# Kernel optimization log

Measured on AMD Instinct MI355X. Metric: run time of the kernel, lower is better.

Reference implementation:

```python
import jax, jax.numpy as jnp
import numpy as np

B, L, H, NH, NB = 8, 200, 128, 4, 2
HD = H // NH
ITEM_NUM, TIME_SPAN = 50000, 256
PAD = -2.0**32 + 1.0


def setup_inputs() -> dict:
    key = jax.random.key(0)
    ks = jax.random.split(key, 32)
    def g(i, shape, s=0.02):
        return jax.random.normal(ks[i], shape, jnp.float32) * s
    item_emb = g(0, (ITEM_NUM + 1, H)).at[0].set(0.0)  # padding_idx=0
    return dict(
        user_ids=jax.random.randint(ks[1], (B,), 0, 1000),
        log_seqs=jax.random.randint(ks[2], (B, L), 0, ITEM_NUM),
        time_matrices=jax.random.randint(ks[3], (B, L, L), 0, TIME_SPAN + 1),
        pos_seqs=jax.random.randint(ks[4], (B, L), 0, ITEM_NUM + 1),
        neg_seqs=jax.random.randint(ks[5], (B, L), 0, ITEM_NUM + 1),
        item_emb=item_emb,
        pos_K_emb=g(6, (L, H)), pos_V_emb=g(7, (L, H)),
        time_K_emb=g(8, (TIME_SPAN + 1, H)), time_V_emb=g(9, (TIME_SPAN + 1, H)),
        attn_ln_g=jnp.ones((NB, H)), attn_ln_b=jnp.zeros((NB, H)),
        Wq=g(10, (NB, H, H)), bq=jnp.zeros((NB, H)),
        Wk=g(11, (NB, H, H)), bk=jnp.zeros((NB, H)),
        Wv=g(12, (NB, H, H)), bv=jnp.zeros((NB, H)),
        fwd_ln_g=jnp.ones((NB, H)), fwd_ln_b=jnp.zeros((NB, H)),
        W1=g(13, (NB, H, H)), b1=jnp.zeros((NB, H)),
        W2=g(14, (NB, H, H)), b2=jnp.zeros((NB, H)),
        last_ln_g=jnp.ones((H,)), last_ln_b=jnp.zeros((H,)),
    )


def _ln(x, g, b, eps=1e-8):
    m = x.mean(-1, keepdims=True)
    v = jnp.var(x, axis=-1, keepdims=True)
    return (x - m) / jnp.sqrt(v + eps) * g + b


def _heads(x):
    # [..., H] -> [NH, ..., HD]; matches torch.cat(torch.split(x, HD, -1), 0)
    y = x.reshape(x.shape[:-1] + (NH, HD))
    return jnp.moveaxis(y, -2, 0)


def reference(user_ids, log_seqs, time_matrices, pos_seqs, neg_seqs, item_emb,
              pos_K_emb, pos_V_emb, time_K_emb, time_V_emb,
              attn_ln_g, attn_ln_b, Wq, bq, Wk, bk, Wv, bv,
              fwd_ln_g, fwd_ln_b, W1, b1, W2, b2, last_ln_g, last_ln_b):
    # user_ids is unused in the original forward as well.
    tmask = log_seqs == 0                                  # [B,L] True = pad
    keep = (~tmask)[..., None].astype(jnp.float32)
    seqs = item_emb[log_seqs] * np.float32(np.sqrt(H))
    seqs = seqs * keep
    pKh = _heads(pos_K_emb)                                # [NH,L,HD]
    pVh = _heads(pos_V_emb)
    tKh = _heads(time_K_emb[time_matrices])                # [NH,B,L,L,HD]
    tVh = _heads(time_V_emb[time_matrices])
    causal = ~jnp.tril(jnp.ones((L, L), bool))             # True above diag -> masked
    bad = tmask[:, :, None] | causal[None]                 # [B,L,L]
    scale = np.float32(np.sqrt(HD))
    for i in range(NB):
        Qin = _ln(seqs, attn_ln_g[i], attn_ln_b[i])
        Qh = _heads(Qin @ Wq[i].T + bq[i])                 # [NH,B,L,HD]
        Kh = _heads(seqs @ Wk[i].T + bk[i])
        Vh = _heads(seqs @ Wv[i].T + bv[i])
        attn = (jnp.einsum('nbqd,nbkd->nbqk', Qh, Kh)
                + jnp.einsum('nbqd,nkd->nbqk', Qh, pKh)
                + jnp.einsum('nbqkd,nbqd->nbqk', tKh, Qh)) / scale
        attn = jnp.where(bad[None], PAD, attn)
        attn = jax.nn.softmax(attn, axis=-1)
        out = (jnp.einsum('nbqk,nbkd->nbqd', attn, Vh)
               + jnp.einsum('nbqk,nkd->nbqd', attn, pVh)
               + jnp.einsum('nbqk,nbqkd->nbqd', attn, tVh))
        out = jnp.moveaxis(out, 0, -2).reshape(seqs.shape)  # merge heads -> [B,L,H]
        seqs = Qin + out                                    # residual uses LN'd Q (as in source)
        seqs = _ln(seqs, fwd_ln_g[i], fwd_ln_b[i])
        ff = jax.nn.relu(seqs @ W1[i].T + b1[i]) @ W2[i].T + b2[i] + seqs
        seqs = ff * keep
    log_feats = _ln(seqs, last_ln_g, last_ln_b)
    pos_logits = (log_feats * item_emb[pos_seqs]).sum(-1)   # [B,L]
    neg_logits = (log_feats * item_emb[neg_seqs]).sum(-1)
    return pos_logits, neg_logits
```

## Files before the change

### kernel.cpp

```cpp
#include <hip/hip_runtime.h>
#include <hip/hip_bf16.h>

#define BB 8
#define LL 200
#define HH 128
#define NHEAD 4
#define HDIM 32
#define NBLK 2
#define BL (BB * LL)
#define NT 257
#define QT 8
#define NQT 25
#define SSP 208
#define KTP 66
#define ASP 36
#define BSP 66
#define FASP 20
#define RSP 132

static constexpr float SQRT_H    = 11.313708498984761f;
static constexpr float INV_SCALE = 0.17677669529663687f;
static constexpr float PADV      = -4294967295.0f;

__global__ void k_qkv_gemm(const float* __restrict__ seqs_in,
                           const int* __restrict__ log_seqs,
                           const float* __restrict__ item_emb,
                           const float* __restrict__ g, const float* __restrict__ bia,
                           const float* __restrict__ Wq, const float* __restrict__ bq,
                           const float* __restrict__ Wk, const float* __restrict__ bk,
                           const float* __restrict__ Wv, const float* __restrict__ bv,
                           const float* __restrict__ posK, const float* __restrict__ posV,
                           float* __restrict__ Qin, float* __restrict__ Q,
                           float* __restrict__ K, float* __restrict__ V) {
    int mt = blockIdx.x / 6, nt = blockIdx.x % 6;
    int matsel = nt >> 1;
    int jb = (nt & 1) * 64;
    int row0 = mt * 32;
    int tid = threadIdx.x;
    __shared__ float As[128 * ASP];
    __shared__ float Bs[128 * BSP];

    {
        int r = tid >> 3, seg = tid & 7;
        int row = row0 + r;
        float4 vv[4];
        if (seqs_in) {
            #pragma unroll
            for (int i = 0; i < 4; i++)
                vv[i] = *(const float4*)(seqs_in + (size_t)row * HH + seg * 16 + i * 4);
        } else {
            int idx = log_seqs[row];
            if (idx == 0) {
                #pragma unroll
                for (int i = 0; i < 4; i++) vv[i] = make_float4(0.f, 0.f, 0.f, 0.f);
            } else {
                #pragma unroll
                for (int i = 0; i < 4; i++) {
                    float4 e = *(const float4*)(item_emb + (size_t)idx * HH + seg * 16 + i * 4);
                    vv[i] = make_float4(e.x * SQRT_H, e.y * SQRT_H, e.z * SQRT_H, e.w * SQRT_H);
                }
            }
        }
        if (matsel == 0) {
            float s = 0.f, s2 = 0.f;
            #pragma unroll
            for (int i = 0; i < 4; i++) {
                s  += vv[i].x + vv[i].y + vv[i].z + vv[i].w;
                s2 += vv[i].x * vv[i].x + vv[i].y * vv[i].y + vv[i].z * vv[i].z + vv[i].w * vv[i].w;
            }
            #pragma unroll
            for (int off = 1; off < 8; off <<= 1) {
                s  += __shfl_xor(s, off);
                s2 += __shfl_xor(s2, off);
            }
            float mean = s * (1.f / HH);
            float var  = s2 * (1.f / HH) - mean * mean;
            float inv  = 1.f / sqrtf(var + 1e-8f);
            #pragma unroll
            for (int i = 0; i < 4; i++) {
                int k = seg * 16 + i * 4;
                float4 g4 = *(const float4*)(g + k);
                float4 b4 = *(const float4*)(bia + k);
                float4 y;
                y.x = (vv[i].x - mean) * inv * g4.x + b4.x;
                y.y = (vv[i].y - mean) * inv * g4.y + b4.y;
                y.z = (vv[i].z - mean) * inv * g4.z + b4.z;
                y.w = (vv[i].w - mean) * inv * g4.w + b4.w;
                As[(k + 0) * ASP + r] = y.x;
                As[(k + 1) * ASP + r] = y.y;
                As[(k + 2) * ASP + r] = y.z;
                As[(k + 3) * ASP + r] = y.w;
                if (nt == 0) *(float4*)(Qin + (size_t)row * HH + k) = y;
            }
        } else {
            #pragma unroll
            for (int i = 0; i < 4; i++) {
                int k = seg * 16 + i * 4;
                As[(k + 0) * ASP + r] = vv[i].x;
                As[(k + 1) * ASP + r] = vv[i].y;
                As[(k + 2) * ASP + r] = vv[i].z;
                As[(k + 3) * ASP + r] = vv[i].w;
            }
        }
    }
    {
        const float* W = (matsel == 0) ? Wq : (matsel == 1) ? Wk : Wv;
        int k4 = tid & 31, jj0 = tid >> 5;
        #pragma unroll
        for (int p = 0; p < 8; p++) {
            int jj = jj0 + p * 8;
            float4 w = *(const float4*)(W + (size_t)(jb + jj) * HH + k4 * 4);
            Bs[(k4 * 4 + 0) * BSP + jj] = w.x;
            Bs[(k4 * 4 + 1) * BSP + jj] = w.y;
            Bs[(k4 * 4 + 2) * BSP + jj] = w.z;
            Bs[(k4 * 4 + 3) * BSP + jj] = w.w;
        }
    }
    __syncthreads();

    int my = tid >> 5, jx = tid & 31;
    float a00=0,a01=0,a10=0,a11=0,a20=0,a21=0,a30=0,a31=0;
    #pragma unroll 4
    for (int k = 0; k < HH; k++) {
        float4 a = *(const float4*)&As[k * ASP + my * 4];
        float2 b = *(const float2*)&Bs[k * BSP + jx * 2];
        a00 += a.x * b.x; a01 += a.x * b.y;
        a10 += a.y * b.x; a11 += a.y * b.y;
        a20 += a.z * b.x; a21 += a.z * b.y;
        a30 += a.w * b.x; a31 += a.w * b.y;
    }
    float accs[4][2] = {{a00,a01},{a10,a11},{a20,a21},{a30,a31}};
    int col = jb + jx * 2;
    if (matsel == 0) {
        float2 bb = *(const float2*)(bq + col);
        #pragma unroll
        for (int r = 0; r < 4; r++) {
            int row = row0 + my * 4 + r;
            float2 o = make_float2((accs[r][0] + bb.x) * INV_SCALE,
                                   (accs[r][1] + bb.y) * INV_SCALE);
            *(float2*)(Q + (size_t)row * HH + col) = o;
        }
    } else if (matsel == 1) {
        float2 bb = *(const float2*)(bk + col);
        #pragma unroll
        for (int r = 0; r < 4; r++) {
            int row = row0 + my * 4 + r;
            int l = row % LL;
            float2 pk = *(const float2*)(posK + (size_t)l * HH + col);
            float2 o = make_float2(accs[r][0] + bb.x + pk.x, accs[r][1] + bb.y + pk.y);
            *(float2*)(K + (size_t)row * HH + col) = o;
        }
    } else {
        float2 bb = *(const float2*)(bv + col);
        #pragma unroll
        for (int r = 0; r < 4; r++) {
            int row = row0 + my * 4 + r;
            int l = row % LL;
            float2 pv = *(const float2*)(posV + (size_t)l * HH + col);
            float2 o = make_float2(accs[r][0] + bb.x + pv.x, accs[r][1] + bb.y + pv.y);
            *(float2*)(V + (size_t)row * HH + col) = o;
        }
    }
}

__global__ void k_attn(const float* __restrict__ Q, const float* __restrict__ K,
                       const float* __restrict__ V,
                       const float* __restrict__ timeK, const float* __restrict__ timeV,
                       const int* __restrict__ tm,
                       float* __restrict__ att) {
    int bn = blockIdx.x & 31;
    int b = bn >> 2, n = bn & 3;
    int qt = (NQT - 1) - (blockIdx.x >> 5);
    int q0 = qt * QT;
    int kmax = q0 + QT - 1;
    int tid = threadIdx.x;
    int wv = tid >> 6, ln = tid & 63;

    __shared__ float Qs[QT * HDIM];
    __shared__ float KstT[HDIM * KTP];
    __shared__ float DTW[QT * NT];
    __shared__ float Ssc[QT * SSP];
    __shared__ int   tmst[QT * LL];
    __shared__ float Ost[QT * HDIM];

    Ost[tid] = 0.f;
    if (tid < 64) {
        int qi = tid >> 3, d4 = tid & 7;
        *(float4*)(Qs + qi * HDIM + d4 * 4) =
            *(const float4*)(Q + ((size_t)(b * LL + q0 + qi)) * HH + n * HDIM + d4 * 4);
    }
    #pragma unroll
    for (int qi = 0; qi < QT; qi++)
        if (tid < LL)
            tmst[qi * LL + tid] = tm[((size_t)(b * LL + q0 + qi)) * LL + tid];
    __syncthreads();

    int k2 = tid & 31, qi_c = tid >> 5;

    for (int c = 0; c < 5; c++) {
        #pragma unroll
        for (int p = 0; p < 2; p++) {
            int idx = tid + p * 256;
            int r = idx >> 3, d4 = idx & 7;
            int tau = c * 64 + r;
            float4 w = make_float4(0.f, 0.f, 0.f, 0.f);
            if (tau < NT) w = *(const float4*)(timeK + (size_t)tau * HH + n * HDIM + d4 * 4);
            KstT[(d4 * 4 + 0) * KTP + r] = w.x;
            KstT[(d4 * 4 + 1) * KTP + r] = w.y;
            KstT[(d4 * 4 + 2) * KTP + r] = w.z;
            KstT[(d4 * 4 + 3) * KTP + r] = w.w;
        }
        __syncthreads();
        float a0 = 0.f, a1 = 0.f;
        #pragma unroll 4
        for (int d = 0; d < HDIM; d++) {
            float qv = Qs[qi_c * HDIM + d];
            float2 kv = *(const float2*)&KstT[d * KTP + k2 * 2];
            a0 += qv * kv.x; a1 += qv * kv.y;
        }
        int tau0 = c * 64 + k2 * 2;
        if (tau0 < NT)     DTW[qi_c * NT + tau0]     = a0;
        if (tau0 + 1 < NT) DTW[qi_c * NT + tau0 + 1] = a1;
        __syncthreads();
    }

    int nch = (kmax >> 6) + 1;
    for (int c = 0; c < nch; c++) {
        #pragma unroll
        for (int p = 0; p < 2; p++) {
            int idx = tid + p * 256;
            int r = idx >> 3, d4 = idx & 7;
            int k = c * 64 + r;
            float4 w = make_float4(0.f, 0.f, 0.f, 0.f);
            if (k < LL) w = *(const float4*)(K + ((size_t)(b * LL + k)) * HH + n * HDIM + d4 * 4);
            KstT[(d4 * 4 + 0) * KTP + r] = w.x;
            KstT[(d4 * 4 + 1) * KTP + r] = w.y;
            KstT[(d4 * 4 + 2) * KTP + r] = w.z;
            KstT[(d4 * 4 + 3) * KTP + r] = w.w;
        }
        __syncthreads();
        float a0 = 0.f, a1 = 0.f;
        #pragma unroll 4
        for (int d = 0; d < HDIM; d++) {
            float qv = Qs[qi_c * HDIM + d];
            float2 kv = *(const float2*)&KstT[d * KTP + k2 * 2];
            a0 += qv * kv.x; a1 += qv * kv.y;
        }
        int q = q0 + qi_c;
        int k0 = c * 64 + k2 * 2;
        if (k0 <= kmax)
            Ssc[qi_c * SSP + k0] = (k0 <= q) ? (a0 + DTW[qi_c * NT + tmst[qi_c * LL + k0]]) : PADV;
        if (k0 + 1 <= kmax)
            Ssc[qi_c * SSP + k0 + 1] = (k0 + 1 <= q) ? (a1 + DTW[qi_c * NT + tmst[qi_c * LL + k0 + 1]]) : PADV;
        __syncthreads();
    }

    for (int idx = tid; idx < QT * NT; idx += 256) DTW[idx] = 0.f;
    __syncthreads();

    for (int rr = 0; rr < 2; rr++) {
        int qi = wv + rr * 4;
        int q = q0 + qi;
        float sv[4];
        float m = PADV;
        #pragma unroll
        for (int jj = 0; jj < 4; jj++) {
            int k = ln + 64 * jj;
            sv[jj] = (k <= q) ? Ssc[qi * SSP + k] : PADV;
            m = fmaxf(m, sv[jj]);
        }
        for (int off = 32; off; off >>= 1) m = fmaxf(m, __shfl_xor(m, off));
        float sum = 0.f;
        #pragma unroll
        for (int jj = 0; jj < 4; jj++) {
            int k = ln + 64 * jj;
            sv[jj] = (k <= q) ? __expf(sv[jj] - m) : 0.f;
            sum += sv[jj];
        }
        for (int off = 32; off; off >>= 1) sum += __shfl_xor(sum, off);
        float inv = 1.f / sum;
        #pragma unroll
        for (int jj = 0; jj < 4; jj++) {
            int k = ln + 64 * jj;
            float p = sv[jj] * inv;
            if (k < SSP) Ssc[qi * SSP + k] = (k <= q) ? p : 0.f;
            if (k <= q) atomicAdd(&DTW[qi * NT + tmst[qi * LL + k]], p);
        }
    }
    __syncthreads();

    int d = tid & 31, kg = tid >> 5;
    float acc[QT] = {0,0,0,0,0,0,0,0};
    const float* vb = V + ((size_t)(b * LL)) * HH + n * HDIM + d;
    for (int k = kg; k <= kmax; k += 8) {
        float v = vb[(size_t)k * HH];
        #pragma unroll
        for (int qi = 0; qi < QT; qi++) acc[qi] += Ssc[qi * SSP + k] * v;
    }
    const float* tvb = timeV + n * HDIM + d;
    for (int t = kg; t < NT; t += 8) {
        float v = tvb[(size_t)t * HH];
        #pragma unroll
        for (int qi = 0; qi < QT; qi++) acc[qi] += DTW[qi * NT + t] * v;
    }
    #pragma unroll
    for (int qi = 0; qi < QT; qi++) atomicAdd(&Ost[qi * HDIM + d], acc[qi]);
    __syncthreads();
    {
        int qi = tid >> 5;
        att[((size_t)(b * LL + q0 + qi)) * HH + n * HDIM + d] = Ost[qi * HDIM + d];
    }
}

__global__ void k_ff1(const float* __restrict__ Qin, const float* __restrict__ att,
                      const float* __restrict__ g, const float* __restrict__ bia,
                      const float* __restrict__ W1, const float* __restrict__ b1,
                      float* __restrict__ h1) {
    int mt = blockIdx.x >> 1, nt = blockIdx.x & 1;
    int jb = nt * 64;
    int row0 = mt * 16;
    int tid = threadIdx.x;
    __shared__ float As[128 * FASP];
    __shared__ float Bs[128 * BSP];

    {
        int r = tid >> 4, seg = tid & 15;
        int row = row0 + r;
        float4 vv[2];
        #pragma unroll
        for (int i = 0; i < 2; i++) {
            int k = seg * 8 + i * 4;
            float4 q4 = *(const float4*)(Qin + (size_t)row * HH + k);
            float4 a4 = *(const float4*)(att + (size_t)row * HH + k);
            vv[i] = make_float4(q4.x + a4.x, q4.y + a4.y, q4.z + a4.z, q4.w + a4.w);
        }
        float s = 0.f, s2 = 0.f;
        #pragma unroll
        for (int i = 0; i < 2; i++) {
            s  += vv[i].x + vv[i].y + vv[i].z + vv[i].w;
            s2 += vv[i].x * vv[i].x + vv[i].y * vv[i].y + vv[i].z * vv[i].z + vv[i].w * vv[i].w;
        }
        #pragma unroll
        for (int off = 1; off < 16; off <<= 1) {
            s  += __shfl_xor(s, off);
            s2 += __shfl_xor(s2, off);
        }
        float mean = s * (1.f / HH);
        float var  = s2 * (1.f / HH) - mean * mean;
        float inv  = 1.f / sqrtf(var + 1e-8f);
        #pragma unroll
        for (int i = 0; i < 2; i++) {
            int k = seg * 8 + i * 4;
            float4 g4 = *(const float4*)(g + k);
            float4 b4 = *(const float4*)(bia + k);
            As[(k + 0) * FASP + r] = (vv[i].x - mean) * inv * g4.x + b4.x;
            As[(k + 1) * FASP + r] = (vv[i].y - mean) * inv * g4.y + b4.y;
            As[(k + 2) * FASP + r] = (vv[i].z - mean) * inv * g4.z + b4.z;
            As[(k + 3) * FASP + r] = (vv[i].w - mean) * inv * g4.w + b4.w;
        }
    }
    {
        int k4 = tid & 31, jj0 = tid >> 5;
        #pragma unroll
        for (int p = 0; p < 8; p++) {
            int jj = jj0 + p * 8;
            float4 w = *(const float4*)(W1 + (size_t)(jb + jj) * HH + k4 * 4);
            Bs[(k4 * 4 + 0) * BSP + jj] = w.x;
            Bs[(k4 * 4 + 1) * BSP + jj] = w.y;
            Bs[(k4 * 4 + 2) * BSP + jj] = w.z;
            Bs[(k4 * 4 + 3) * BSP + jj] = w.w;
        }
    }
    __syncthreads();

    int my = tid >> 5, jx = tid & 31;
    float a00 = 0, a01 = 0, a10 = 0, a11 = 0;
    #pragma unroll 4
    for (int k = 0; k < HH; k++) {
        float2 a = *(const float2*)&As[k * FASP + my * 2];
        float2 b = *(const float2*)&Bs[k * BSP + jx * 2];
        a00 += a.x * b.x; a01 += a.x * b.y;
        a10 += a.y * b.x; a11 += a.y * b.y;
    }
    int col = jb + jx * 2;
    float2 bb = *(const float2*)(b1 + col);
    {
        int row = row0 + my * 2;
        float2 o0 = make_float2(fmaxf(a00 + bb.x, 0.f), fmaxf(a01 + bb.y, 0.f));
        float2 o1 = make_float2(fmaxf(a10 + bb.x, 0.f), fmaxf(a11 + bb.y, 0.f));
        *(float2*)(h1 + (size_t)row * HH + col) = o0;
        *(float2*)(h1 + (size_t)(row + 1) * HH + col) = o1;
    }
}

__global__ void k_ff2(const float* __restrict__ h1,
                      const float* __restrict__ Qin, const float* __restrict__ att,
                      const float* __restrict__ g, const float* __restrict__ bia,
                      const float* __restrict__ W2, const float* __restrict__ b2,
                      const int* __restrict__ log_seqs,
                      float* __restrict__ out) {
    int mt = blockIdx.x >> 1, nt = blockIdx.x & 1;
    int jb = nt * 64;
    int row0 = mt * 16;
    int tid = threadIdx.x;
    __shared__ float As[128 * FASP];
    __shared__ float Bs[128 * BSP];
    __shared__ float Rs[16 * RSP];
    __shared__ float mu[16], rstd[16];

    {
        int r = tid >> 4, seg = tid & 15;
        int row = row0 + r;
        #pragma unroll
        for (int i = 0; i < 2; i++) {
            int k = seg * 8 + i * 4;
            float4 h4 = *(const float4*)(h1 + (size_t)row * HH + k);
            As[(k + 0) * FASP + r] = h4.x;
            As[(k + 1) * FASP + r] = h4.y;
            As[(k + 2) * FASP + r] = h4.z;
            As[(k + 3) * FASP + r] = h4.w;
        }
        float s = 0.f, s2 = 0.f;
        #pragma unroll
        for (int i = 0; i < 2; i++) {
            int k = seg * 8 + i * 4;
            float4 q4 = *(const float4*)(Qin + (size_t)row * HH + k);
            float4 a4 = *(const float4*)(att + (size_t)row * HH + k);
            float4 v = make_float4(q4.x + a4.x, q4.y + a4.y, q4.z + a4.z, q4.w + a4.w);
            *(float4*)(Rs + r * RSP + k) = v;
            s  += v.x + v.y + v.z + v.w;
            s2 += v.x * v.x + v.y * v.y + v.z * v.z + v.w * v.w;
        }
        #pragma unroll
        for (int off = 1; off < 16; off <<= 1) {
            s  += __shfl_xor(s, off);
            s2 += __shfl_xor(s2, off);
        }
        float mean = s * (1.f / HH);
        float var  = s2 * (1.f / HH) - mean * mean;
        if (seg == 0) { mu[r] = mean; rstd[r] = 1.f / sqrtf(var + 1e-8f); }
    }
    {
        int k4 = tid & 31, jj0 = tid >> 5;
        #pragma unroll
        for (int p = 0; p < 8; p++) {
            int jj = jj0 + p * 8;
            float4 w = *(const float4*)(W2 + (size_t)(jb + jj) * HH + k4 * 4);
            Bs[(k4 * 4 + 0) * BSP + jj] = w.x;
            Bs[(k4 * 4 + 1) * BSP + jj] = w.y;
            Bs[(k4 * 4 + 2) * BSP + jj] = w.z;
            Bs[(k4 * 4 + 3) * BSP + jj] = w.w;
        }
    }
    __syncthreads();

    int my = tid >> 5, jx = tid & 31;
    float a00 = 0, a01 = 0, a10 = 0, a11 = 0;
    #pragma unroll 4
    for (int k = 0; k < HH; k++) {
        float2 a = *(const float2*)&As[k * FASP + my * 2];
        float2 b = *(const float2*)&Bs[k * BSP + jx * 2];
        a00 += a.x * b.x; a01 += a.x * b.y;
        a10 += a.y * b.x; a11 += a.y * b.y;
    }
    int col = jb + jx * 2;
    float2 bb = *(const float2*)(b2 + col);
    float2 g2 = *(const float2*)(g + col);
    float2 lb = *(const float2*)(bia + col);
    float accs[2][2] = {{a00, a01}, {a10, a11}};
    #pragma unroll
    for (int r = 0; r < 2; r++) {
        int ri = my * 2 + r;
        int row = row0 + ri;
        float m = mu[ri], iv = rstd[ri];
        float2 R = *(const float2*)&Rs[ri * RSP + col];
        float y0 = (R.x - m) * iv * g2.x + lb.x;
        float y1 = (R.y - m) * iv * g2.y + lb.y;
        float2 o = make_float2(accs[r][0] + bb.x + y0, accs[r][1] + bb.y + y1);
        if (log_seqs[row] == 0) o = make_float2(0.f, 0.f);
        *(float2*)(out + (size_t)row * HH + col) = o;
    }
}

__global__ void k_lnlogits(const float* __restrict__ seqs,
                           const float* __restrict__ g, const float* __restrict__ bia,
                           const float* __restrict__ item_emb,
                           const int* __restrict__ pos, const int* __restrict__ neg,
                           float* __restrict__ out) {
    int row = blockIdx.x;
    int h = threadIdx.x;
    float v = seqs[(size_t)row * HH + h];
    float s = v, s2 = v * v;
    for (int off = 32; off; off >>= 1) {
        s  += __shfl_xor(s, off);
        s2 += __shfl_xor(s2, off);
    }
    __shared__ float r1[2], r2[2];
    if ((h & 63) == 0) { r1[h >> 6] = s; r2[h >> 6] = s2; }
    __syncthreads();
    float mean = (r1[0] + r1[1]) * (1.f / HH);
    float var  = (r2[0] + r2[1]) * (1.f / HH) - mean * mean;
    float inv = 1.f / sqrtf(var + 1e-8f);
    float f = (v - mean) * inv * g[h] + bia[h];

    int ip = pos[row], in_ = neg[row];
    float vp = f * item_emb[(size_t)ip * HH + h];
    float vn = f * item_emb[(size_t)in_ * HH + h];
    for (int off = 32; off; off >>= 1) {
        vp += __shfl_xor(vp, off);
        vn += __shfl_xor(vn, off);
    }
    __shared__ float rp[2], rn[2];
    if ((h & 63) == 0) { rp[h >> 6] = vp; rn[h >> 6] = vn; }
    __syncthreads();
    if (h == 0) {
        out[row]      = rp[0] + rp[1];
        out[BL + row] = rn[0] + rn[1];
    }
}

extern "C" void kernel_launch(void* const* d_in, const int* in_sizes, int n_in,
                              void* d_out, int out_size, void* d_ws, size_t ws_size,
                              hipStream_t stream) {
    const int* log_seqs   = (const int*)d_in[1];
    const int* tm         = (const int*)d_in[2];
    const int* pos_seqs   = (const int*)d_in[3];
    const int* neg_seqs   = (const int*)d_in[4];
    const float* item_emb = (const float*)d_in[5];
    const float* posK     = (const float*)d_in[6];
    const float* posV     = (const float*)d_in[7];
    const float* timeK    = (const float*)d_in[8];
    const float* timeV    = (const float*)d_in[9];
    const float* attn_g   = (const float*)d_in[10];
    const float* attn_b   = (const float*)d_in[11];
    const float* Wq       = (const float*)d_in[12];
    const float* bq       = (const float*)d_in[13];
    const float* Wk       = (const float*)d_in[14];
    const float* bk       = (const float*)d_in[15];
    const float* Wv       = (const float*)d_in[16];
    const float* bv       = (const float*)d_in[17];
    const float* fwd_g    = (const float*)d_in[18];
    const float* fwd_b    = (const float*)d_in[19];
    const float* W1       = (const float*)d_in[20];
    const float* b1       = (const float*)d_in[21];
    const float* W2       = (const float*)d_in[22];
    const float* b2       = (const float*)d_in[23];
    const float* last_g   = (const float*)d_in[24];
    const float* last_b   = (const float*)d_in[25];

    float* seqs = (float*)d_ws;
    float* Qin  = seqs + (size_t)BL * HH;
    float* Qb   = Qin  + (size_t)BL * HH;
    float* Kb   = Qb   + (size_t)BL * HH;
    float* Vb   = Kb   + (size_t)BL * HH;
    float* att  = Vb   + (size_t)BL * HH;
    float* h1   = att  + (size_t)BL * HH;

    for (int i = 0; i < NBLK; i++) {
        k_qkv_gemm<<<300, 256, 0, stream>>>(i == 0 ? nullptr : seqs, log_seqs, item_emb,
                                            attn_g + i * HH, attn_b + i * HH,
                                            Wq + (size_t)i * HH * HH, bq + i * HH,
                                            Wk + (size_t)i * HH * HH, bk + i * HH,
                                            Wv + (size_t)i * HH * HH, bv + i * HH,
                                            posK, posV, Qin, Qb, Kb, Vb);
        k_attn<<<NQT * 32, 256, 0, stream>>>(Qb, Kb, Vb, timeK, timeV, tm, att);
        k_ff1<<<200, 256, 0, stream>>>(Qin, att, fwd_g + i * HH, fwd_b + i * HH,
                                       W1 + (size_t)i * HH * HH, b1 + i * HH, h1);
        k_ff2<<<200, 256, 0, stream>>>(h1, Qin, att, fwd_g + i * HH, fwd_b + i * HH,
                                       W2 + (size_t)i * HH * HH, b2 + i * HH,
                                       log_seqs, seqs);
    }
    k_lnlogits<<<BL, HH, 0, stream>>>(seqs, last_g, last_b, item_emb,
                                      pos_seqs, neg_seqs, (float*)d_out);
}
```

Baseline: 241.0 us.

## Fuse FFN layers and final logits into one kernel; restructure attention time-bias handling

Merges k_ff1, k_ff2 and the final layernorm/logits kernel into a single k_ffn kernel that keeps the hidden activation in shared memory, processing 4 rows per block. This removes the h1 round trip and two launches. The attention kernel widens its K tiles to 128 columns with float4 reads and stores time indices as ushort. It now gathers timeV rows per (q,k) directly instead of scattering probabilities into time buckets with shared atomics. The fused FFN reloads W1/W2 into shared memory for every 4-row block (400 blocks), so it does more weight traffic per row, and the direct timeV gathers add global loads.

```diff
diff --git a/kernel.cpp b/kernel.cpp
--- a/kernel.cpp
+++ b/kernel.cpp
@@ -12,11 +12,10 @@
 #define QT 8
 #define NQT 25
 #define SSP 208
-#define KTP 66
+#define KC 132
 #define ASP 36
 #define BSP 66
-#define FASP 20
-#define RSP 132
+#define FSP 132
 
 static constexpr float SQRT_H    = 11.313708498984761f;
 static constexpr float INV_SCALE = 0.17677669529663687f;
@@ -147,8 +146,8 @@
             int row = row0 + my * 4 + r;
             int l = row % LL;
             float2 pk = *(const float2*)(posK + (size_t)l * HH + col);
-            float2 o = make_float2(accs[r][0] + bb.x + pk.x, accs[r][1] + bb.y + pk.y);
-            *(float2*)(K + (size_t)row * HH + col) = o;
+            *(float2*)(K + (size_t)row * HH + col) =
+                make_float2(accs[r][0] + bb.x + pk.x, accs[r][1] + bb.y + pk.y);
         }
     } else {
         float2 bb = *(const float2*)(bv + col);
@@ -157,8 +156,8 @@
             int row = row0 + my * 4 + r;
             int l = row % LL;
             float2 pv = *(const float2*)(posV + (size_t)l * HH + col);
-            float2 o = make_float2(accs[r][0] + bb.x + pv.x, accs[r][1] + bb.y + pv.y);
-            *(float2*)(V + (size_t)row * HH + col) = o;
+            *(float2*)(V + (size_t)row * HH + col) =
+                make_float2(accs[r][0] + bb.x + pv.x, accs[r][1] + bb.y + pv.y);
         }
     }
 }
@@ -177,10 +176,10 @@
     int wv = tid >> 6, ln = tid & 63;
 
     __shared__ float Qs[QT * HDIM];
-    __shared__ float KstT[HDIM * KTP];
+    __shared__ float KstT[HDIM * KC];
     __shared__ float DTW[QT * NT];
     __shared__ float Ssc[QT * SSP];
-    __shared__ int   tmst[QT * LL];
+    __shared__ unsigned short tmst[QT * LL];
     __shared__ float Ost[QT * HDIM];
 
     Ost[tid] = 0.f;
@@ -189,84 +188,92 @@
         *(float4*)(Qs + qi * HDIM + d4 * 4) =
             *(const float4*)(Q + ((size_t)(b * LL + q0 + qi)) * HH + n * HDIM + d4 * 4);
     }
-    #pragma unroll
-    for (int qi = 0; qi < QT; qi++)
-        if (tid < LL)
-            tmst[qi * LL + tid] = tm[((size_t)(b * LL + q0 + qi)) * LL + tid];
+    for (int idx = tid; idx < QT * LL; idx += 256) {
+        int qi = idx / LL, k = idx - qi * LL;
+        tmst[idx] = (unsigned short)tm[((size_t)(b * LL + q0 + qi)) * LL + k];
+    }
     __syncthreads();
 
-    int k2 = tid & 31, qi_c = tid >> 5;
-
-    for (int c = 0; c < 5; c++) {
-        #pragma unroll
-        for (int p = 0; p < 2; p++) {
+    int qi_c = tid >> 5, k2 = tid & 31;
+
+    for (int c = 0; c < 2; c++) {
+        int base = c * 128, rows = c ? 129 : 128;
+        #pragma unroll
+        for (int p = 0; p < 5; p++) {
             int idx = tid + p * 256;
             int r = idx >> 3, d4 = idx & 7;
-            int tau = c * 64 + r;
-            float4 w = make_float4(0.f, 0.f, 0.f, 0.f);
-            if (tau < NT) w = *(const float4*)(timeK + (size_t)tau * HH + n * HDIM + d4 * 4);
-            KstT[(d4 * 4 + 0) * KTP + r] = w.x;
-            KstT[(d4 * 4 + 1) * KTP + r] = w.y;
-            KstT[(d4 * 4 + 2) * KTP + r] = w.z;
-            KstT[(d4 * 4 + 3) * KTP + r] = w.w;
-        }
-        __syncthreads();
-        float a0 = 0.f, a1 = 0.f;
-        #pragma unroll 4
+            if (r < rows) {
+                float4 w = *(const float4*)(timeK + (size_t)(base + r) * HH + n * HDIM + d4 * 4);
+                KstT[(d4 * 4 + 0) * KC + r] = w.x;
+                KstT[(d4 * 4 + 1) * KC + r] = w.y;
+                KstT[(d4 * 4 + 2) * KC + r] = w.z;
+                KstT[(d4 * 4 + 3) * KC + r] = w.w;
+            }
+        }
+        __syncthreads();
+        float a0 = 0, a1 = 0, a2 = 0, a3 = 0;
+        int col = k2 * 4;
+        #pragma unroll 8
         for (int d = 0; d < HDIM; d++) {
             float qv = Qs[qi_c * HDIM + d];
-            float2 kv = *(const float2*)&KstT[d * KTP + k2 * 2];
-            a0 += qv * kv.x; a1 += qv * kv.y;
-        }
-        int tau0 = c * 64 + k2 * 2;
-        if (tau0 < NT)     DTW[qi_c * NT + tau0]     = a0;
-        if (tau0 + 1 < NT) DTW[qi_c * NT + tau0 + 1] = a1;
-        __syncthreads();
-    }
-
-    int nch = (kmax >> 6) + 1;
+            float4 kv = *(const float4*)&KstT[d * KC + col];
+            a0 += qv * kv.x; a1 += qv * kv.y; a2 += qv * kv.z; a3 += qv * kv.w;
+        }
+        float* dt = &DTW[qi_c * NT + base + col];
+        dt[0] = a0; dt[1] = a1; dt[2] = a2; dt[3] = a3;
+        if (c == 1 && k2 == 0) {
+            float a = 0.f;
+            #pragma unroll 8
+            for (int d = 0; d < HDIM; d++) a += Qs[qi_c * HDIM + d] * KstT[d * KC + 128];
+            DTW[qi_c * NT + 256] = a;
+        }
+        __syncthreads();
+    }
+
+    int nch = (kmax >> 7) + 1;
     for (int c = 0; c < nch; c++) {
-        #pragma unroll
-        for (int p = 0; p < 2; p++) {
+        int base = c * 128;
+        int rows = min(128, kmax + 1 - base);
+        #pragma unroll
+        for (int p = 0; p < 4; p++) {
             int idx = tid + p * 256;
             int r = idx >> 3, d4 = idx & 7;
-            int k = c * 64 + r;
-            float4 w = make_float4(0.f, 0.f, 0.f, 0.f);
-            if (k < LL) w = *(const float4*)(K + ((size_t)(b * LL + k)) * HH + n * HDIM + d4 * 4);
-            KstT[(d4 * 4 + 0) * KTP + r] = w.x;
-            KstT[(d4 * 4 + 1) * KTP + r] = w.y;
-            KstT[(d4 * 4 + 2) * KTP + r] = w.z;
-            KstT[(d4 * 4 + 3) * KTP + r] = w.w;
-        }
-        __syncthreads();
-        float a0 = 0.f, a1 = 0.f;
-        #pragma unroll 4
+            if (r < rows) {
+                float4 w = *(const float4*)(K + ((size_t)(b * LL + base + r)) * HH + n * HDIM + d4 * 4);
+                KstT[(d4 * 4 + 0) * KC + r] = w.x;
+                KstT[(d4 * 4 + 1) * KC + r] = w.y;
+                KstT[(d4 * 4 + 2) * KC + r] = w.z;
+                KstT[(d4 * 4 + 3) * KC + r] = w.w;
+            }
+        }
+        __syncthreads();
+        float av[4] = {0, 0, 0, 0};
+        int col = k2 * 4;
+        #pragma unroll 8
         for (int d = 0; d < HDIM; d++) {
             float qv = Qs[qi_c * HDIM + d];
-            float2 kv = *(const float2*)&KstT[d * KTP + k2 * 2];
-            a0 += qv * kv.x; a1 += qv * kv.y;
+            float4 kv = *(const float4*)&KstT[d * KC + col];
+            av[0] += qv * kv.x; av[1] += qv * kv.y; av[2] += qv * kv.z; av[3] += qv * kv.w;
         }
         int q = q0 + qi_c;
-        int k0 = c * 64 + k2 * 2;
-        if (k0 <= kmax)
-            Ssc[qi_c * SSP + k0] = (k0 <= q) ? (a0 + DTW[qi_c * NT + tmst[qi_c * LL + k0]]) : PADV;
-        if (k0 + 1 <= kmax)
-            Ssc[qi_c * SSP + k0 + 1] = (k0 + 1 <= q) ? (a1 + DTW[qi_c * NT + tmst[qi_c * LL + k0 + 1]]) : PADV;
-        __syncthreads();
-    }
-
-    for (int idx = tid; idx < QT * NT; idx += 256) DTW[idx] = 0.f;
-    __syncthreads();
+        #pragma unroll
+        for (int j = 0; j < 4; j++) {
+            int k = base + col + j;
+            if (k <= q)
+                Ssc[qi_c * SSP + k] = av[j] + DTW[qi_c * NT + tmst[qi_c * LL + k]];
+        }
+        __syncthreads();
+    }
 
     for (int rr = 0; rr < 2; rr++) {
         int qi = wv + rr * 4;
         int q = q0 + qi;
         float sv[4];
-        float m = PADV;
+        float m = -3.0e38f;
         #pragma unroll
         for (int jj = 0; jj < 4; jj++) {
             int k = ln + 64 * jj;
-            sv[jj] = (k <= q) ? Ssc[qi * SSP + k] : PADV;
+            sv[jj] = (k <= q) ? Ssc[qi * SSP + k] : -3.0e38f;
             m = fmaxf(m, sv[jj]);
         }
         for (int off = 32; off; off >>= 1) m = fmaxf(m, __shfl_xor(m, off));
@@ -282,240 +289,142 @@
         #pragma unroll
         for (int jj = 0; jj < 4; jj++) {
             int k = ln + 64 * jj;
-            float p = sv[jj] * inv;
-            if (k < SSP) Ssc[qi * SSP + k] = (k <= q) ? p : 0.f;
-            if (k <= q) atomicAdd(&DTW[qi * NT + tmst[qi * LL + k]], p);
+            if (k <= q) Ssc[qi * SSP + k] = sv[jj] * inv;
         }
     }
     __syncthreads();
 
     int d = tid & 31, kg = tid >> 5;
     float acc[QT] = {0,0,0,0,0,0,0,0};
-    const float* vb = V + ((size_t)(b * LL)) * HH + n * HDIM + d;
+    const float* vb  = V + ((size_t)(b * LL)) * HH + n * HDIM + d;
+    const float* tvb = timeV + n * HDIM + d;
     for (int k = kg; k <= kmax; k += 8) {
         float v = vb[(size_t)k * HH];
         #pragma unroll
-        for (int qi = 0; qi < QT; qi++) acc[qi] += Ssc[qi * SSP + k] * v;
-    }
-    const float* tvb = timeV + n * HDIM + d;
-    for (int t = kg; t < NT; t += 8) {
-        float v = tvb[(size_t)t * HH];
-        #pragma unroll
-        for (int qi = 0; qi < QT; qi++) acc[qi] += DTW[qi * NT + t] * v;
+        for (int qi = 0; qi < QT; qi++) {
+            if (q0 + qi >= k) {
+                float tv = tvb[(size_t)tmst[qi * LL + k] * HH];
+                acc[qi] += Ssc[qi * SSP + k] * (v + tv);
+            }
+        }
     }
     #pragma unroll
-    for (int qi = 0; qi < QT; qi++) atomicAdd(&Ost[qi * HDIM + d], acc[qi]);
+    for (int qi = 0; qi < QT; qi++) {
+        acc[qi] += __shfl_xor(acc[qi], 32);
+        if ((kg & 1) == 0) atomicAdd(&Ost[qi * HDIM + d], acc[qi]);
+    }
     __syncthreads();
     {
         int qi = tid >> 5;
-        att[((size_t)(b * LL + q0 + qi)) * HH + n * HDIM + d] = Ost[qi * HDIM + d];
+        att[((size_t)(b * LL + q0 + qi)) * HH + n * HDIM + (tid & 31)] = Ost[tid];
     }
 }
 
-__global__ void k_ff1(const float* __restrict__ Qin, const float* __restrict__ att,
+__global__ void k_ffn(const float* __restrict__ Qin, const float* __restrict__ att,
                       const float* __restrict__ g, const float* __restrict__ bia,
                       const float* __restrict__ W1, const float* __restrict__ b1,
-                      float* __restrict__ h1) {
-    int mt = blockIdx.x >> 1, nt = blockIdx.x & 1;
-    int jb = nt * 64;
-    int row0 = mt * 16;
+                      const float* __restrict__ W2, const float* __restrict__ b2,
+                      const int* __restrict__ log_seqs,
+                      const float* __restrict__ lg, const float* __restrict__ lb,
+                      const float* __restrict__ item_emb,
+                      const int* __restrict__ pos, const int* __restrict__ neg,
+                      float* __restrict__ out, float* __restrict__ logits, int last) {
+    int row0 = blockIdx.x * 4;
     int tid = threadIdx.x;
-    __shared__ float As[128 * FASP];
+    int wv = tid >> 6, ln = tid & 63;
+    __shared__ float As[4 * FSP];
+    __shared__ float H1[4 * FSP];
     __shared__ float Bs[128 * BSP];
 
     {
-        int r = tid >> 4, seg = tid & 15;
-        int row = row0 + r;
-        float4 vv[2];
-        #pragma unroll
-        for (int i = 0; i < 2; i++) {
-            int k = seg * 8 + i * 4;
-            float4 q4 = *(const float4*)(Qin + (size_t)row * HH + k);
-            float4 a4 = *(const float4*)(att + (size_t)row * HH + k);
-            vv[i] = make_float4(q4.x + a4.x, q4.y + a4.y, q4.z + a4.z, q4.w + a4.w);
-        }
-        float s = 0.f, s2 = 0.f;
-        #pragma unroll
-        for (int i = 0; i < 2; i++) {
-            s  += vv[i].x + vv[i].y + vv[i].z + vv[i].w;
-            s2 += vv[i].x * vv[i].x + vv[i].y * vv[i].y + vv[i].z * vv[i].z + vv[i].w * vv[i].w;
-        }
-        #pragma unroll
-        for (int off = 1; off < 16; off <<= 1) {
+        int row = row0 + wv;
+        float v0 = Qin[(size_t)row * HH + ln]      + att[(size_t)row * HH + ln];
+        float v1 = Qin[(size_t)row * HH + ln + 64] + att[(size_t)row * HH + ln + 64];
+        float s = v0 + v1, s2 = v0 * v0 + v1 * v1;
+        for (int off = 32; off; off >>= 1) {
             s  += __shfl_xor(s, off);
             s2 += __shfl_xor(s2, off);
         }
         float mean = s * (1.f / HH);
         float var  = s2 * (1.f / HH) - mean * mean;
         float inv  = 1.f / sqrtf(var + 1e-8f);
-        #pragma unroll
-        for (int i = 0; i < 2; i++) {
-            int k = seg * 8 + i * 4;
-            float4 g4 = *(const float4*)(g + k);
-            float4 b4 = *(const float4*)(bia + k);
-            As[(k + 0) * FASP + r] = (vv[i].x - mean) * inv * g4.x + b4.x;
-            As[(k + 1) * FASP + r] = (vv[i].y - mean) * inv * g4.y + b4.y;
-            As[(k + 2) * FASP + r] = (vv[i].z - mean) * inv * g4.z + b4.z;
-            As[(k + 3) * FASP + r] = (vv[i].w - mean) * inv * g4.w + b4.w;
-        }
-    }
-    {
+        As[wv * FSP + ln]      = (v0 - mean) * inv * g[ln]      + bia[ln];
+        As[wv * FSP + ln + 64] = (v1 - mean) * inv * g[ln + 64] + bia[ln + 64];
+    }
+    __syncthreads();
+
+    int jx = ln;
+    for (int c = 0; c < 2; c++) {
         int k4 = tid & 31, jj0 = tid >> 5;
         #pragma unroll
         for (int p = 0; p < 8; p++) {
             int jj = jj0 + p * 8;
-            float4 w = *(const float4*)(W1 + (size_t)(jb + jj) * HH + k4 * 4);
+            float4 w = *(const float4*)(W1 + (size_t)(c * 64 + jj) * HH + k4 * 4);
             Bs[(k4 * 4 + 0) * BSP + jj] = w.x;
             Bs[(k4 * 4 + 1) * BSP + jj] = w.y;
             Bs[(k4 * 4 + 2) * BSP + jj] = w.z;
             Bs[(k4 * 4 + 3) * BSP + jj] = w.w;
         }
-    }
-    __syncthreads();
-
-    int my = tid >> 5, jx = tid & 31;
-    float a00 = 0, a01 = 0, a10 = 0, a11 = 0;
-    #pragma unroll 4
-    for (int k = 0; k < HH; k++) {
-        float2 a = *(const float2*)&As[k * FASP + my * 2];
-        float2 b = *(const float2*)&Bs[k * BSP + jx * 2];
-        a00 += a.x * b.x; a01 += a.x * b.y;
-        a10 += a.y * b.x; a11 += a.y * b.y;
-    }
-    int col = jb + jx * 2;
-    float2 bb = *(const float2*)(b1 + col);
-    {
-        int row = row0 + my * 2;
-        float2 o0 = make_float2(fmaxf(a00 + bb.x, 0.f), fmaxf(a01 + bb.y, 0.f));
-        float2 o1 = make_float2(fmaxf(a10 + bb.x, 0.f), fmaxf(a11 + bb.y, 0.f));
-        *(float2*)(h1 + (size_t)row * HH + col) = o0;
-        *(float2*)(h1 + (size_t)(row + 1) * HH + col) = o1;
-    }
-}
-
-__global__ void k_ff2(const float* __restrict__ h1,
-                      const float* __restrict__ Qin, const float* __restrict__ att,
-                      const float* __restrict__ g, const float* __restrict__ bia,
-                      const float* __restrict__ W2, const float* __restrict__ b2,
-                      const int* __restrict__ log_seqs,
-                      float* __restrict__ out) {
-    int mt = blockIdx.x >> 1, nt = blockIdx.x & 1;
-    int jb = nt * 64;
-    int row0 = mt * 16;
-    int tid = threadIdx.x;
-    __shared__ float As[128 * FASP];
-    __shared__ float Bs[128 * BSP];
-    __shared__ float Rs[16 * RSP];
-    __shared__ float mu[16], rstd[16];
-
-    {
-        int r = tid >> 4, seg = tid & 15;
-        int row = row0 + r;
-        #pragma unroll
-        for (int i = 0; i < 2; i++) {
-            int k = seg * 8 + i * 4;
-            float4 h4 = *(const float4*)(h1 + (size_t)row * HH + k);
-            As[(k + 0) * FASP + r] = h4.x;
-            As[(k + 1) * FASP + r] = h4.y;
-            As[(k + 2) * FASP + r] = h4.z;
-            As[(k + 3) * FASP + r] = h4.w;
-        }
-        float s = 0.f, s2 = 0.f;
-        #pragma unroll
-        for (int i = 0; i < 2; i++) {
-            int k = seg * 8 + i * 4;
-            float4 q4 = *(const float4*)(Qin + (size_t)row * HH + k);
-            float4 a4 = *(const float4*)(att + (size_t)row * HH + k);
-            float4 v = make_float4(q4.x + a4.x, q4.y + a4.y, q4.z + a4.z, q4.w + a4.w);
-            *(float4*)(Rs + r * RSP + k) = v;
-            s  += v.x + v.y + v.z + v.w;
-            s2 += v.x * v.x + v.y * v.y + v.z * v.z + v.w * v.w;
-        }
-        #pragma unroll
-        for (int off = 1; off < 16; off <<= 1) {
-            s  += __shfl_xor(s, off);
-            s2 += __shfl_xor(s2, off);
-        }
-        float mean = s * (1.f / HH);
-        float var  = s2 * (1.f / HH) - mean * mean;
-        if (seg == 0) { mu[r] = mean; rstd[r] = 1.f / sqrtf(var + 1e-8f); }
-    }
-    {
+        __syncthreads();
+        float acc = 0.f;
+        #pragma unroll 8
+        for (int k = 0; k < HH; k++)
+            acc += As[wv * FSP + k] * Bs[k * BSP + jx];
+        int col = c * 64 + jx;
+        float t = acc + b1[col];
+        H1[wv * FSP + col] = t > 0.f ? t : 0.f;
+        __syncthreads();
+    }
+
+    int rowm = row0 + wv;
+    int keepz = (log_seqs[rowm] == 0);
+    for (int c = 0; c < 2; c++) {
         int k4 = tid & 31, jj0 = tid >> 5;
         #pragma unroll
         for (int p = 0; p < 8; p++) {
             int jj = jj0 + p * 8;
-            float4 w = *(const float4*)(W2 + (size_t)(jb + jj) * HH + k4 * 4);
+            float4 w = *(const float4*)(W2 + (size_t)(c * 64 + jj) * HH + k4 * 4);
             Bs[(k4 * 4 + 0) * BSP + jj] = w.x;
             Bs[(k4 * 4 + 1) * BSP + jj] = w.y;
             Bs[(k4 * 4 + 2) * BSP + jj] = w.z;
             Bs[(k4 * 4 + 3) * BSP + jj] = w.w;
         }
-    }
-    __syncthreads();
-
-    int my = tid >> 5, jx = tid & 31;
-    float a00 = 0, a01 = 0, a10 = 0, a11 = 0;
-    #pragma unroll 4
-    for (int k = 0; k < HH; k++) {
-        float2 a = *(const float2*)&As[k * FASP + my * 2];
-        float2 b = *(const float2*)&Bs[k * BSP + jx * 2];
-        a00 += a.x * b.x; a01 += a.x * b.y;
-        a10 += a.y * b.x; a11 += a.y * b.y;
-    }
-    int col = jb + jx * 2;
-    float2 bb = *(const float2*)(b2 + col);
-    float2 g2 = *(const float2*)(g + col);
-    float2 lb = *(const float2*)(bia + col);
-    float accs[2][2] = {{a00, a01}, {a10, a11}};
-    #pragma unroll
-    for (int r = 0; r < 2; r++) {
-        int ri = my * 2 + r;
-        int row = row0 + ri;
-        float m = mu[ri], iv = rstd[ri];
-        float2 R = *(const float2*)&Rs[ri * RSP + col];
-        float y0 = (R.x - m) * iv * g2.x + lb.x;
-        float y1 = (R.y - m) * iv * g2.y + lb.y;
-        float2 o = make_float2(accs[r][0] + bb.x + y0, accs[r][1] + bb.y + y1);
-        if (log_seqs[row] == 0) o = make_float2(0.f, 0.f);
-        *(float2*)(out + (size_t)row * HH + col) = o;
-    }
-}
-
-__global__ void k_lnlogits(const float* __restrict__ seqs,
-                           const float* __restrict__ g, const float* __restrict__ bia,
-                           const float* __restrict__ item_emb,
-                           const int* __restrict__ pos, const int* __restrict__ neg,
-                           float* __restrict__ out) {
-    int row = blockIdx.x;
-    int h = threadIdx.x;
-    float v = seqs[(size_t)row * HH + h];
-    float s = v, s2 = v * v;
-    for (int off = 32; off; off >>= 1) {
-        s  += __shfl_xor(s, off);
-        s2 += __shfl_xor(s2, off);
-    }
-    __shared__ float r1[2], r2[2];
-    if ((h & 63) == 0) { r1[h >> 6] = s; r2[h >> 6] = s2; }
-    __syncthreads();
-    float mean = (r1[0] + r1[1]) * (1.f / HH);
-    float var  = (r2[0] + r2[1]) * (1.f / HH) - mean * mean;
-    float inv = 1.f / sqrtf(var + 1e-8f);
-    float f = (v - mean) * inv * g[h] + bia[h];
-
-    int ip = pos[row], in_ = neg[row];
-    float vp = f * item_emb[(size_t)ip * HH + h];
-    float vn = f * item_emb[(size_t)in_ * HH + h];
-    for (int off = 32; off; off >>= 1) {
-        vp += __shfl_xor(vp, off);
-        vn += __shfl_xor(vn, off);
-    }
-    __shared__ float rp[2], rn[2];
-    if ((h & 63) == 0) { rp[h >> 6] = vp; rn[h >> 6] = vn; }
-    __syncthreads();
-    if (h == 0) {
-        out[row]      = rp[0] + rp[1];
-        out[BL + row] = rn[0] + rn[1];
+        __syncthreads();
+        float acc = 0.f;
+        #pragma unroll 8
+        for (int k = 0; k < HH; k++)
+            acc += H1[wv * FSP + k] * Bs[k * BSP + jx];
+        int col = c * 64 + jx;
+        float o = acc + b2[col] + As[wv * FSP + col];
+        if (keepz) o = 0.f;
+        if (!last) out[(size_t)rowm * HH + col] = o;
+        As[wv * FSP + col] = o;
+        __syncthreads();
+    }
+
+    if (last) {
+        float o0 = As[wv * FSP + ln], o1 = As[wv * FSP + ln + 64];
+        float s = o0 + o1, s2 = o0 * o0 + o1 * o1;
+        for (int off = 32; off; off >>= 1) {
+            s  += __shfl_xor(s, off);
+            s2 += __shfl_xor(s2, off);
+        }
+        float mean = s * (1.f / HH);
+        float var  = s2 * (1.f / HH) - mean * mean;
+        float inv  = 1.f / sqrtf(var + 1e-8f);
+        float f0 = (o0 - mean) * inv * lg[ln]      + lb[ln];
+        float f1 = (o1 - mean) * inv * lg[ln + 64] + lb[ln + 64];
+        int ip = pos[rowm], in_ = neg[rowm];
+        float vp = f0 * item_emb[(size_t)ip * HH + ln] + f1 * item_emb[(size_t)ip * HH + ln + 64];
+        float vn = f0 * item_emb[(size_t)in_ * HH + ln] + f1 * item_emb[(size_t)in_ * HH + ln + 64];
+        for (int off = 32; off; off >>= 1) {
+            vp += __shfl_xor(vp, off);
+            vn += __shfl_xor(vn, off);
+        }
+        if (ln == 0) {
+            logits[rowm]      = vp;
+            logits[BL + rowm] = vn;
+        }
     }
 }
 
@@ -554,7 +463,6 @@
     float* Kb   = Qb   + (size_t)BL * HH;
     float* Vb   = Kb   + (size_t)BL * HH;
     float* att  = Vb   + (size_t)BL * HH;
-    float* h1   = att  + (size_t)BL * HH;
 
     for (int i = 0; i < NBLK; i++) {
         k_qkv_gemm<<<300, 256, 0, stream>>>(i == 0 ? nullptr : seqs, log_seqs, item_emb,
@@ -564,12 +472,11 @@
                                             Wv + (size_t)i * HH * HH, bv + i * HH,
                                             posK, posV, Qin, Qb, Kb, Vb);
         k_attn<<<NQT * 32, 256, 0, stream>>>(Qb, Kb, Vb, timeK, timeV, tm, att);
-        k_ff1<<<200, 256, 0, stream>>>(Qin, att, fwd_g + i * HH, fwd_b + i * HH,
-                                       W1 + (size_t)i * HH * HH, b1 + i * HH, h1);
-        k_ff2<<<200, 256, 0, stream>>>(h1, Qin, att, fwd_g + i * HH, fwd_b + i * HH,
-                                       W2 + (size_t)i * HH * HH, b2 + i * HH,
-                                       log_seqs, seqs);
-    }
-    k_lnlogits<<<BL, HH, 0, stream>>>(seqs, last_g, last_b, item_emb,
-                                      pos_seqs, neg_seqs, (float*)d_out);
+        k_ffn<<<BL / 4, 256, 0, stream>>>(Qin, att, fwd_g + i * HH, fwd_b + i * HH,
+                                          W1 + (size_t)i * HH * HH, b1 + i * HH,
+                                          W2 + (size_t)i * HH * HH, b2 + i * HH,
+                                          log_seqs, last_g, last_b, item_emb,
+                                          pos_seqs, neg_seqs,
+                                          seqs, (float*)d_out, (i == NBLK - 1) ? 1 : 0);
+    }
 }
```

New measurement: 258.2 us. +7.1%, slower.
